# Performance work log

Hardware: AMD Instinct MI355X
Metric: run time of the kernel (lower is better)

Reference implementation:

```python
import jax, jax.numpy as jnp
import numpy as np

N_NODES = 20000

def _gcn_conv(x, W, b, src, dst, n):
    # PyG GCNConv: add self-loops, symmetric normalization D^-1/2 (A+I) D^-1/2, then XW + b
    h = x @ W                                   # [n, out]
    loop = jnp.arange(n, dtype=src.dtype)
    s = jnp.concatenate([src, loop])            # sources incl. self-loops
    d = jnp.concatenate([dst, loop])            # targets incl. self-loops
    deg = jax.ops.segment_sum(jnp.ones_like(d, dtype=h.dtype), d, num_segments=n)
    dinv = jnp.where(deg > 0, jax.lax.rsqrt(deg), 0.0)
    norm = dinv[s] * dinv[d]                    # [E+n]
    msg = h[s] * norm[:, None]                  # gather + scale
    out = jax.ops.segment_sum(msg, d, num_segments=n)  # scatter-add
    return out + b


def setup_inputs() -> dict:
    key = jax.random.key(0)
    ks = jax.random.split(key, 12)
    n, text_dim, hidden, ncls = N_NODES, 768, 128, 4
    mel_flat = 128 * 128
    E = 640000
    def lin(k, fan_in, fan_out):
        bound = 1.0 / np.sqrt(fan_in)
        kw, kb = jax.random.split(k)
        W = jax.random.uniform(kw, (fan_in, fan_out), jnp.float32, -bound, bound)
        b = jax.random.uniform(kb, (fan_out,), jnp.float32, -bound, bound)
        return W, b
    W_mel, b_mel = lin(ks[0], mel_flat, hidden)
    W_cat, b_cat = lin(ks[1], text_dim + hidden, hidden)
    W1, b1 = lin(ks[2], hidden, hidden)
    W2, b2 = lin(ks[3], hidden, ncls)
    return {
        "text": jax.random.normal(ks[4], (n, text_dim), jnp.float32),
        "mel": jax.random.normal(ks[5], (n, 128, 128), jnp.float32),
        "edge_index": jax.random.randint(ks[6], (2, E), 0, n, jnp.int32),
        "W_mel": W_mel, "b_mel": b_mel,
        "W_cat": W_cat, "b_cat": b_cat,
        "W1": W1, "b1": b1,
        "W2": W2, "b2": b2,
    }


def reference(text, mel, edge_index, W_mel, b_mel, W_cat, b_cat, W1, b1, W2, b2):
    n = text.shape[0]
    src, dst = edge_index[0], edge_index[1]
    m = mel.reshape(n, -1)                      # flatten [N, 128*128]
    m = jax.nn.relu(m @ W_mel + b_mel)          # [N, hidden]
    x = jnp.concatenate([text, m], axis=1)      # [N, text_dim + hidden]
    x = jax.nn.relu(x @ W_cat + b_cat)          # [N, hidden]
    x = jax.nn.relu(_gcn_conv(x, W1, b1, src, dst, n))
    x = _gcn_conv(x, W2, b2, src, dst, n)       # [N, num_classes]
    return x
```

## Files before the change

kernel.cpp:

```cpp
#include <hip/hip_runtime.h>
#include <hip/hip_bf16.h>
#include <cstdint>

typedef float f32x4 __attribute__((ext_vector_type(4)));
typedef __bf16 bf16x8 __attribute__((ext_vector_type(8)));
typedef __bf16 bf16x4 __attribute__((ext_vector_type(4)));
typedef __bf16 bf16x2 __attribute__((ext_vector_type(2)));

#define HID 128

__global__ void count_pack(const int* __restrict__ dstI, int* __restrict__ cnt, int E,
                           const float* __restrict__ Wa, const float* __restrict__ Wb,
                           const float* __restrict__ Wc,
                           __bf16* __restrict__ Ba, __bf16* __restrict__ Bb,
                           __bf16* __restrict__ Bc) {
    if (blockIdx.x < 256) {
        for (int e = blockIdx.x * 256 + threadIdx.x; e < E; e += 65536)
            atomicAdd(&cnt[dstI[e]], 1);
        return;
    }
    int idx = (blockIdx.x - 256) * 256 + threadIdx.x;
    const int T1 = 512 * 512;
    const int T2 = 28 * 512;
    const float* W; __bf16* B; int li;
    if (idx < T1)            { W = Wa; B = Ba; li = idx; }
    else if (idx < T1 + T2)  { W = Wb; B = Bb; li = idx - T1; }
    else                     { W = Wc; B = Bc; li = idx - T1 - T2; }
    int lane = li & 63;
    int nf = (li >> 6) & 7;
    int ki = li >> 9;
    int n = nf * 16 + (lane & 15);
    int kb = ki * 32 + ((lane >> 4) * 8);
    bf16x8 v;
#pragma unroll
    for (int j = 0; j < 8; ++j) v[j] = (__bf16)W[(size_t)(kb + j) * HID + n];
    *reinterpret_cast<bf16x8*>(B + (size_t)li * 8) = v;
}

__global__ __launch_bounds__(256, 2) void gemm_mel_fill(
    const float* __restrict__ A0,
    const __bf16* __restrict__ Bf,
    __bf16* __restrict__ part,
    const int* __restrict__ srcI, const int* __restrict__ dstI,
    const int* __restrict__ offs, int* __restrict__ cnt,
    int* __restrict__ srcs, int E)
{
    const int b = blockIdx.x;
    if ((b % 11) == 10) {
        int fid = b / 11;
        for (int e = fid * 256 + threadIdx.x; e < E; e += 64000) {
            int d = dstI[e];
            int p = offs[d] + atomicAdd(&cnt[d], -1) - 1;
            srcs[p] = srcI[e];
        }
        return;
    }
    const int bid = b - b / 11;
    const int tid = threadIdx.x;
    const int lane = tid & 63;
    const int wv = tid >> 6;
    const int quarter = bid / 625;
    const int row_base = (bid - quarter * 625) * 32;
    const int rif = lane & 15;
    const int kg = lane >> 4;
    const int s0 = quarter * 8;

    __shared__ __align__(16) char ldsb[65536];

    f32x4 zero = {0.f, 0.f, 0.f, 0.f};
    f32x4 acc[2][8];
#pragma unroll
    for (int i = 0; i < 2; ++i)
#pragma unroll
        for (int j = 0; j < 8; ++j) acc[i][j] = zero;

    const bf16x8* __restrict__ BfV = reinterpret_cast<const bf16x8*>(Bf);

    f32x4 st[16];

    auto stage_load = [&](int s) {
#pragma unroll
        for (int j = 0; j < 16; ++j) {
            int seg = wv * 16 + j;
            int row = seg >> 1, halfseg = seg & 1;
            const float* gp = A0 + (size_t)(row_base + row) * 16384 + s * 512 + halfseg * 256 + (lane << 2);
            st[j] = __builtin_nontemporal_load(reinterpret_cast<const f32x4*>(gp));
        }
    };
    auto stage_write = [&](int buf) {
#pragma unroll
        for (int j = 0; j < 16; ++j) {
            int seg = wv * 16 + j;
            int row = seg >> 1, halfseg = seg & 1;
            int byte = row * 1024 + ((halfseg * 512 + lane * 8) ^ ((row & 7) << 4)) + buf * 32768;
            bf16x4 v;
            v[0] = (__bf16)st[j][0]; v[1] = (__bf16)st[j][1];
            v[2] = (__bf16)st[j][2]; v[3] = (__bf16)st[j][3];
            *reinterpret_cast<bf16x4*>(ldsb + byte) = v;
        }
    };
    auto compute2 = [&](int cur, int s, int kt0) {
#pragma unroll
        for (int kt = kt0; kt < kt0 + 2; ++kt) {
            bf16x8 af[2];
#pragma unroll
            for (int mi = 0; mi < 2; ++mi) {
                int row = mi * 16 + rif;
                int byte = row * 1024 + ((wv * 256 + kt * 64 + kg * 16) ^ ((rif & 7) << 4)) + cur * 32768;
                af[mi] = *reinterpret_cast<const bf16x8*>(ldsb + byte);
            }
            int ki = s * 16 + wv * 4 + kt;
            const bf16x8* bp = BfV + (size_t)ki * 512 + lane;
#pragma unroll
            for (int nf = 0; nf < 8; ++nf) {
                bf16x8 bq = bp[nf * 64];
                acc[0][nf] = __builtin_amdgcn_mfma_f32_16x16x32_bf16(af[0], bq, acc[0][nf], 0, 0, 0);
                acc[1][nf] = __builtin_amdgcn_mfma_f32_16x16x32_bf16(af[1], bq, acc[1][nf], 0, 0, 0);
            }
        }
    };

    stage_load(s0);
    stage_write(0);
    for (int t = 0; t < 8; ++t) {
        int s = s0 + t;
        int cur = t & 1;
        if (t + 1 < 8) stage_load(s + 1);
        __syncthreads();
        compute2(cur, s, 0);
        compute2(cur, s, 2);
        if (t + 1 < 8) stage_write(cur ^ 1);
    }

    __syncthreads();
    float* red = reinterpret_cast<float*>(ldsb);
#pragma unroll
    for (int mi = 0; mi < 2; ++mi)
#pragma unroll
        for (int nf = 0; nf < 8; ++nf)
#pragma unroll
            for (int j = 0; j < 4; ++j)
                red[(wv * 32 + mi * 16 + kg * 4 + j) * HID + nf * 16 + rif] = acc[mi][nf][j];
    __syncthreads();
    __bf16* pb = part + (size_t)quarter * 20000 * HID;
#pragma unroll
    for (int p = 0; p < 8; ++p) {
        int idx = tid + p * 256;
        int r = idx >> 6;
        int c2 = (idx & 63) * 2;
        float v0 = red[r * HID + c2]     + red[(32 + r) * HID + c2]
                 + red[(64 + r) * HID + c2] + red[(96 + r) * HID + c2];
        float v1 = red[r * HID + c2 + 1] + red[(32 + r) * HID + c2 + 1]
                 + red[(64 + r) * HID + c2 + 1] + red[(96 + r) * HID + c2 + 1];
        union { bf16x2 h; unsigned int u; } cv;
        cv.h[0] = (__bf16)v0; cv.h[1] = (__bf16)v1;
        __builtin_nontemporal_store(cv.u,
            reinterpret_cast<unsigned int*>(pb + (size_t)(row_base + r) * HID + c2));
    }
}

__global__ __launch_bounds__(256) void gemm_cat_h1(
    const float* __restrict__ A0,
    const __bf16* __restrict__ part,
    const float* __restrict__ bmel,
    const __bf16* __restrict__ Bf2,
    const __bf16* __restrict__ Bf3,
    const float* __restrict__ bcat,
    const float* __restrict__ dinv,
    __bf16* __restrict__ h1)
{
    const int tid = threadIdx.x;
    const int lane = tid & 63;
    const int w = tid >> 6;
    const int row_base = blockIdx.x * 32;
    const int rif = lane & 15;
    const int kg = lane >> 4;

    f32x4 zero = {0.f, 0.f, 0.f, 0.f};
    f32x4 acc[2][8];
#pragma unroll
    for (int i = 0; i < 2; ++i)
#pragma unroll
        for (int j = 0; j < 8; ++j) acc[i][j] = zero;

    const bf16x8* __restrict__ Bf2V = reinterpret_cast<const bf16x8*>(Bf2);
    const int kstart = w * 224;
    const size_t N = (size_t)20000 * HID;

#pragma unroll
    for (int it = 0; it < 7; ++it) {
        const int k0 = kstart + it * 32;
        const int kc = k0 + kg * 8;
        bf16x8 af[2];
#pragma unroll
        for (int mi = 0; mi < 2; ++mi) {
            const int row = row_base + mi * 16 + rif;
            if (k0 < 768) {
                const f32x4* apv = reinterpret_cast<const f32x4*>(A0 + (size_t)row * 768 + kc);
                f32x4 v0 = __builtin_nontemporal_load(apv);
                f32x4 v1 = __builtin_nontemporal_load(apv + 1);
                af[mi][0] = (__bf16)v0.x; af[mi][1] = (__bf16)v0.y;
                af[mi][2] = (__bf16)v0.z; af[mi][3] = (__bf16)v0.w;
                af[mi][4] = (__bf16)v1.x; af[mi][5] = (__bf16)v1.y;
                af[mi][6] = (__bf16)v1.z; af[mi][7] = (__bf16)v1.w;
            } else {
                const int mcol = kc - 768;
                const size_t base = (size_t)row * HID + mcol;
                bf16x8 q0 = *reinterpret_cast<const bf16x8*>(part + base);
                bf16x8 q1 = *reinterpret_cast<const bf16x8*>(part + N + base);
                bf16x8 q2 = *reinterpret_cast<const bf16x8*>(part + 2 * N + base);
                bf16x8 q3 = *reinterpret_cast<const bf16x8*>(part + 3 * N + base);
                const float* bp_ = bmel + mcol;
#pragma unroll
                for (int jj = 0; jj < 8; ++jj) {
                    float v = (float)q0[jj] + (float)q1[jj] + (float)q2[jj] + (float)q3[jj] + bp_[jj];
                    af[mi][jj] = (__bf16)fmaxf(v, 0.f);
                }
            }
        }
        const bf16x8* bp = Bf2V + (size_t)(k0 >> 5) * 512 + lane;
#pragma unroll
        for (int nf = 0; nf < 8; ++nf) {
            bf16x8 bq = bp[nf * 64];
            acc[0][nf] = __builtin_amdgcn_mfma_f32_16x16x32_bf16(af[0], bq, acc[0][nf], 0, 0, 0);
            acc[1][nf] = __builtin_amdgcn_mfma_f32_16x16x32_bf16(af[1], bq, acc[1][nf], 0, 0, 0);
        }
    }

    __shared__ float red[4][32][HID];
    __shared__ __bf16 xs[32][136];

#pragma unroll
    for (int mi = 0; mi < 2; ++mi)
#pragma unroll
        for (int nf = 0; nf < 8; ++nf)
#pragma unroll
            for (int j = 0; j < 4; ++j)
                red[w][mi * 16 + kg * 4 + j][nf * 16 + rif] = acc[mi][nf][j];
    __syncthreads();
#pragma unroll
    for (int p = 0; p < 16; ++p) {
        int idx = tid + p * 256;
        int r = idx >> 7, c = idx & 127;
        float v = red[0][r][c] + red[1][r][c] + red[2][r][c] + red[3][r][c];
        v = fmaxf(v + bcat[c], 0.f);
        xs[r][c] = (__bf16)v;
    }
    __syncthreads();

    f32x4 acc2[2][8];
#pragma unroll
    for (int i = 0; i < 2; ++i)
#pragma unroll
        for (int j = 0; j < 8; ++j) acc2[i][j] = zero;

    {
        const int k0 = w * 32;
        bf16x8 af[2];
#pragma unroll
        for (int mi = 0; mi < 2; ++mi)
            af[mi] = *reinterpret_cast<const bf16x8*>(&xs[mi * 16 + rif][k0 + kg * 8]);
        const bf16x8* bp = reinterpret_cast<const bf16x8*>(Bf3) + (size_t)w * 512 + lane;
#pragma unroll
        for (int nf = 0; nf < 8; ++nf) {
            bf16x8 bq = bp[nf * 64];
            acc2[0][nf] = __builtin_amdgcn_mfma_f32_16x16x32_bf16(af[0], bq, acc2[0][nf], 0, 0, 0);
            acc2[1][nf] = __builtin_amdgcn_mfma_f32_16x16x32_bf16(af[1], bq, acc2[1][nf], 0, 0, 0);
        }
    }

#pragma unroll
    for (int mi = 0; mi < 2; ++mi)
#pragma unroll
        for (int nf = 0; nf < 8; ++nf)
#pragma unroll
            for (int j = 0; j < 4; ++j)
                red[w][mi * 16 + kg * 4 + j][nf * 16 + rif] = acc2[mi][nf][j];
    __syncthreads();
#pragma unroll
    for (int p = 0; p < 16; ++p) {
        int idx = tid + p * 256;
        int r = idx >> 7, c = idx & 127;
        float v = red[0][r][c] + red[1][r][c] + red[2][r][c] + red[3][r][c];
        h1[(size_t)(row_base + r) * HID + c] = (__bf16)(v * dinv[row_base + r]);
    }
}

__global__ __launch_bounds__(1024) void scan_block(const int* __restrict__ cnt,
    int* __restrict__ offs, float* __restrict__ dinv, int n) {
    int tid = threadIdx.x;
    int CH = (n + 1023) >> 10;
    int s0 = tid * CH;
    int s1 = min(s0 + CH, n);
    int sum = 0;
    for (int i = s0; i < s1; ++i) sum += cnt[i];
    int lane = tid & 63, wv = tid >> 6;
    int s = sum;
#pragma unroll
    for (int off = 1; off < 64; off <<= 1) {
        int t = __shfl_up(s, off);
        if (lane >= off) s += t;
    }
    __shared__ int wsum[16];
    __shared__ int wbase[16];
    if (lane == 63) wsum[wv] = s;
    __syncthreads();
    if (tid == 0) {
        int a = 0;
#pragma unroll
        for (int k = 0; k < 16; ++k) { wbase[k] = a; a += wsum[k]; }
        offs[n] = a;
    }
    __syncthreads();
    int run = wbase[wv] + (s - sum);
    for (int i = s0; i < s1; ++i) {
        int v = cnt[i];
        offs[i] = run;
        dinv[i] = rsqrtf((float)(v + 1));
        run += v;
    }
}

__global__ __launch_bounds__(64) void agg_h_w2(const __bf16* __restrict__ hs,
    const float* __restrict__ dinv, const int* __restrict__ offs,
    const int* __restrict__ srcs,
    const float* __restrict__ b1, const float* __restrict__ W2,
    float* __restrict__ h2, int n) {
    int i = blockIdx.x;
    int c = threadIdx.x;
    float di = dinv[i];
    const int col = 2 * c;
    bf16x2 hv = *reinterpret_cast<const bf16x2*>(hs + (size_t)i * HID + col);
    float a0 = (float)hv[0];
    float a1 = (float)hv[1];
    int o = offs[i];
    int e = offs[i + 1] - o;
    int t = 0;
    for (; t + 8 <= e; t += 8) {
        int sx[8];
#pragma unroll
        for (int q = 0; q < 8; ++q) sx[q] = srcs[o + t + q];
        bf16x2 v[8];
#pragma unroll
        for (int q = 0; q < 8; ++q) v[q] = *reinterpret_cast<const bf16x2*>(hs + (size_t)sx[q] * HID + col);
#pragma unroll
        for (int q = 0; q < 8; ++q) { a0 += (float)v[q][0]; a1 += (float)v[q][1]; }
    }
    for (; t < e; ++t) {
        int s = srcs[o + t];
        bf16x2 v = *reinterpret_cast<const bf16x2*>(hs + (size_t)s * HID + col);
        a0 += (float)v[0];
        a1 += (float)v[1];
    }
    float yb0 = fmaxf(a0 * di + b1[col], 0.f);
    float yb1 = fmaxf(a1 * di + b1[col + 1], 0.f);
    float4 w0 = *reinterpret_cast<const float4*>(W2 + col * 4);
    float4 w1 = *reinterpret_cast<const float4*>(W2 + col * 4 + 4);
    float p0 = yb0 * w0.x + yb1 * w1.x;
    float p1 = yb0 * w0.y + yb1 * w1.y;
    float p2 = yb0 * w0.z + yb1 * w1.z;
    float p3 = yb0 * w0.w + yb1 * w1.w;
#pragma unroll
    for (int off = 32; off; off >>= 1) {
        p0 += __shfl_down(p0, off);
        p1 += __shfl_down(p1, off);
        p2 += __shfl_down(p2, off);
        p3 += __shfl_down(p3, off);
    }
    if (c == 0) {
        float4 r = {p0 * di, p1 * di, p2 * di, p3 * di};
        *reinterpret_cast<float4*>(h2 + (size_t)i * 4) = r;
    }
}

__global__ void agg4(const float* __restrict__ h2s, const float* __restrict__ dinv,
                     const int* __restrict__ offs,
                     const int* __restrict__ srcs, const float* __restrict__ b2,
                     float* __restrict__ out, int n) {
    int gid = blockIdx.x * 256 + threadIdx.x;
    int i = gid >> 2;
    int c = gid & 3;
    if (i >= n) return;
    float di = dinv[i];
    float acc = h2s[(size_t)i * 4 + c];
    int o = offs[i];
    int e = offs[i + 1] - o;
    int t = 0;
    for (; t + 4 <= e; t += 4) {
        int a0 = srcs[o + t], a1 = srcs[o + t + 1], a2 = srcs[o + t + 2], a3 = srcs[o + t + 3];
        acc += h2s[(size_t)a0 * 4 + c] + h2s[(size_t)a1 * 4 + c]
             + h2s[(size_t)a2 * 4 + c] + h2s[(size_t)a3 * 4 + c];
    }
    for (; t < e; ++t) {
        int s = srcs[o + t];
        acc += h2s[(size_t)s * 4 + c];
    }
    out[(size_t)i * 4 + c] = acc * di + b2[c];
}

extern "C" void kernel_launch(void* const* d_in, const int* in_sizes, int n_in,
                              void* d_out, int out_size, void* d_ws, size_t ws_size,
                              hipStream_t stream) {
    const float* text = (const float*)d_in[0];
    const float* mel  = (const float*)d_in[1];
    const int*   ei   = (const int*)d_in[2];
    const float* Wmel = (const float*)d_in[3];
    const float* bmel = (const float*)d_in[4];
    const float* Wcat = (const float*)d_in[5];
    const float* bcat = (const float*)d_in[6];
    const float* W1   = (const float*)d_in[7];
    const float* b1   = (const float*)d_in[8];
    const float* W2   = (const float*)d_in[9];
    const float* b2   = (const float*)d_in[10];
    float* out = (float*)d_out;

    const int n = in_sizes[0] / 768;
    const int E = in_sizes[2] / 2;
    const int Kmel = 16384;

    char* ws = (char*)d_ws;
    size_t off = 0;
    auto alloc = [&](size_t bytes) {
        void* p = ws + off;
        off += (bytes + 255) & ~(size_t)255;
        return p;
    };
    __bf16* Bf1 = (__bf16*)alloc((size_t)Kmel * HID * 2);
    __bf16* Bf2 = (__bf16*)alloc((size_t)896 * HID * 2);
    __bf16* Bf3 = (__bf16*)alloc((size_t)HID * HID * 2);
    __bf16* part = (__bf16*)alloc((size_t)4 * n * HID * 2);
    __bf16* h1  = (__bf16*)alloc((size_t)n * HID * 2);
    float* h2   = (float*)alloc((size_t)n * 4 * 4);
    int* cnt    = (int*)alloc((size_t)n * 4);
    int* offs   = (int*)alloc((size_t)(n + 1) * 4);
    float* dinv = (float*)alloc((size_t)n * 4);
    int* srcs   = (int*)alloc((size_t)E * 4);
    (void)ws_size; (void)n_in; (void)out_size;

    const int* srcI = ei;
    const int* dstI = ei + E;

    (void)hipMemsetAsync(cnt, 0, n * 4, stream);
    count_pack<<<1344, 256, 0, stream>>>(dstI, cnt, E, Wmel, Wcat, W1, Bf1, Bf2, Bf3);
    scan_block<<<1, 1024, 0, stream>>>(cnt, offs, dinv, n);
    gemm_mel_fill<<<2750, 256, 0, stream>>>(mel, Bf1, part, srcI, dstI, offs, cnt, srcs, E);
    gemm_cat_h1<<<n / 32, 256, 0, stream>>>(text, part, bmel, Bf2, Bf3, bcat, dinv, h1);
    agg_h_w2<<<n, 64, 0, stream>>>(h1, dinv, offs, srcs, b1, W2, h2, n);
    agg4<<<(n * 4 + 255) / 256, 256, 0, stream>>>(h2, dinv, offs, srcs, b2, out, n);
}
```

Baseline: 420.8 us.

## Stream fp32 mel tiles straight into LDS with global_load_lds, convert at read

The mel GEMM previously loaded fp32 tiles into registers, converted them to bf16 and wrote them to LDS. It now uses direct global-to-LDS loads of the raw fp32 data, with the swizzle applied on the global address side. The fp32 to bf16 conversion moves to the point where MFMA operands are read from LDS. Because fp32 tiles take twice the space, each stage covers half as much K and the loop runs 16 stages instead of 8. The aim is to free registers and VALU work and overlap the load of the next stage with compute. The cost is more barriers, more LDS traffic per FLOP, and conversion work repeated inside the compute loop.

```diff
diff --git a/kernel.cpp b/kernel.cpp
--- a/kernel.cpp
+++ b/kernel.cpp
@@ -63,7 +63,7 @@
     const int row_base = (bid - quarter * 625) * 32;
     const int rif = lane & 15;
     const int kg = lane >> 4;
-    const int s0 = quarter * 8;
+    const int s0 = quarter * 16;
 
     __shared__ __align__(16) char ldsb[65536];
 
@@ -76,41 +76,39 @@
 
     const bf16x8* __restrict__ BfV = reinterpret_cast<const bf16x8*>(Bf);
 
-    f32x4 st[16];
-
-    auto stage_load = [&](int s) {
-#pragma unroll
-        for (int j = 0; j < 16; ++j) {
-            int seg = wv * 16 + j;
-            int row = seg >> 1, halfseg = seg & 1;
-            const float* gp = A0 + (size_t)(row_base + row) * 16384 + s * 512 + halfseg * 256 + (lane << 2);
-            st[j] = __builtin_nontemporal_load(reinterpret_cast<const f32x4*>(gp));
+    auto issue_loads = [&](int s_abs, int buf) {
+#pragma unroll
+        for (int j = 0; j < 8; ++j) {
+            int row = wv * 8 + j;
+            unsigned sw = (unsigned)((row & 7) << 4);
+            const char* g = reinterpret_cast<const char*>(
+                                A0 + (size_t)(row_base + row) * 16384 + (size_t)s_abs * 256)
+                            + (((unsigned)(lane * 16)) ^ sw);
+            __builtin_amdgcn_global_load_lds(
+                (const __attribute__((address_space(1))) void*)g,
+                (__attribute__((address_space(3))) void*)(ldsb + buf * 32768 + row * 1024),
+                16, 0, 0);
         }
     };
-    auto stage_write = [&](int buf) {
-#pragma unroll
-        for (int j = 0; j < 16; ++j) {
-            int seg = wv * 16 + j;
-            int row = seg >> 1, halfseg = seg & 1;
-            int byte = row * 1024 + ((halfseg * 512 + lane * 8) ^ ((row & 7) << 4)) + buf * 32768;
-            bf16x4 v;
-            v[0] = (__bf16)st[j][0]; v[1] = (__bf16)st[j][1];
-            v[2] = (__bf16)st[j][2]; v[3] = (__bf16)st[j][3];
-            *reinterpret_cast<bf16x4*>(ldsb + byte) = v;
-        }
-    };
-    auto compute2 = [&](int cur, int s, int kt0) {
-#pragma unroll
-        for (int kt = kt0; kt < kt0 + 2; ++kt) {
+    auto compute = [&](int cur, int s_abs) {
+#pragma unroll
+        for (int ki2 = 0; ki2 < 2; ++ki2) {
+            const int ki = wv * 2 + ki2;
             bf16x8 af[2];
 #pragma unroll
             for (int mi = 0; mi < 2; ++mi) {
                 int row = mi * 16 + rif;
-                int byte = row * 1024 + ((wv * 256 + kt * 64 + kg * 16) ^ ((rif & 7) << 4)) + cur * 32768;
-                af[mi] = *reinterpret_cast<const bf16x8*>(ldsb + byte);
+                unsigned sw = (unsigned)((row & 7) << 4);
+                unsigned g0 = (unsigned)(ki * 128 + kg * 32);
+                const char* base = ldsb + cur * 32768 + row * 1024;
+                f32x4 lo = *reinterpret_cast<const f32x4*>(base + (g0 ^ sw));
+                f32x4 hi = *reinterpret_cast<const f32x4*>(base + ((g0 + 16) ^ sw));
+                af[mi][0] = (__bf16)lo.x; af[mi][1] = (__bf16)lo.y;
+                af[mi][2] = (__bf16)lo.z; af[mi][3] = (__bf16)lo.w;
+                af[mi][4] = (__bf16)hi.x; af[mi][5] = (__bf16)hi.y;
+                af[mi][6] = (__bf16)hi.z; af[mi][7] = (__bf16)hi.w;
             }
-            int ki = s * 16 + wv * 4 + kt;
-            const bf16x8* bp = BfV + (size_t)ki * 512 + lane;
+            const bf16x8* bp = BfV + (size_t)(s_abs * 8 + ki) * 512 + lane;
 #pragma unroll
             for (int nf = 0; nf < 8; ++nf) {
                 bf16x8 bq = bp[nf * 64];
@@ -120,19 +118,15 @@
         }
     };
 
-    stage_load(s0);
-    stage_write(0);
-    for (int t = 0; t < 8; ++t) {
-        int s = s0 + t;
+    issue_loads(s0, 0);
+    __syncthreads();
+    for (int t = 0; t < 16; ++t) {
         int cur = t & 1;
-        if (t + 1 < 8) stage_load(s + 1);
+        if (t + 1 < 16) issue_loads(s0 + t + 1, cur ^ 1);
+        compute(cur, s0 + t);
         __syncthreads();
-        compute2(cur, s, 0);
-        compute2(cur, s, 2);
-        if (t + 1 < 8) stage_write(cur ^ 1);
-    }
-
-    __syncthreads();
+    }
+
     float* red = reinterpret_cast<float*>(ldsb);
 #pragma unroll
     for (int mi = 0; mi < 2; ++mi)
```

Measured after the change: 502.7 us. +19.5%, slower.
